# Kernel optimization log

Measured on AMD Instinct MI355X. Metric: run time of the kernel, lower is better.

## Reference

```python
import jax, jax.numpy as jnp
import numpy as np

N, E, F_IN, H, EF, G, GFD = 50000, 800000, 64, 128, 8, 10, 2
NEG_SLOPE = 0.2  # PyG GATv2Conv default negative_slope


def _gatv2_layer(x, src, dst, edge_attr, Wl, bl, Wr, br, We, att, bias):
    # PyG GATv2Conv, heads=1, concat=True, share_weights=False
    n = x.shape[0]
    xl = x @ Wl + bl            # source transform [N,H]
    xr = x @ Wr + br            # target transform [N,H]
    e = edge_attr @ We          # edge embedding   [E,H]
    s = jax.nn.leaky_relu(xl[src] + xr[dst] + e, NEG_SLOPE)  # [E,H]
    logits = s @ att            # [E]
    # numerically-stable segment softmax over destination nodes
    mx = jax.ops.segment_max(logits, dst, num_segments=n)
    mx = jnp.where(jnp.isfinite(mx), mx, 0.0)
    ex = jnp.exp(logits - mx[dst])
    den = jax.ops.segment_sum(ex, dst, num_segments=n)
    alpha = ex / jnp.maximum(den[dst], 1e-16)
    out = jax.ops.segment_sum(alpha[:, None] * xl[src], dst, num_segments=n)
    return out + bias


def _forward(x, edge_index, edge_attr, graph_features, num_graphs, params, head_W, head_b):
    src, dst = edge_index[0], edge_index[1]
    for (Wl, bl, Wr, br, We, att, bias) in params:
        x = jax.nn.relu(_gatv2_layer(x, src, dst, edge_attr, Wl, bl, Wr, br, We, att, bias))
        # dropout p=0.0 / eval mode: no-op
    n_nodes = x.shape[0] // num_graphs
    # faithful replication of the torch reshape chain (graph_feature_dim == 2):
    # graph_features.T [GFD,G] -> unsqueeze(2) -> repeat to [GFD,G,Np] -> view(G,GFD,Np)
    # -> cat(unbind(0), dim=1) -> [GFD, G*Np]
    gf = jnp.broadcast_to(graph_features.T[:, :, None], (GFD, num_graphs, n_nodes))
    gf = gf.reshape(num_graphs, GFD, n_nodes)
    gf = gf.transpose(1, 0, 2).reshape(GFD, num_graphs * n_nodes)
    x = jnp.concatenate([x, gf.T], axis=1)  # [N, H+GFD]
    return x @ head_W + head_b


def setup_inputs():
    key = jax.random.key(0)
    ks = list(jax.random.split(key, 32))
    p = lambda k, s: jax.random.normal(k, s, jnp.float32) * 0.05
    inp = {
        'x': jax.random.normal(ks[0], (N, F_IN), jnp.float32),
        'edge_index': jax.random.randint(ks[1], (2, E), 0, N),
        'edge_attr': jax.random.normal(ks[2], (E, EF), jnp.float32),
        'graph_features': jax.random.normal(ks[3], (G, GFD), jnp.float32),
        'num_graphs': G,
    }
    i = 4
    for l in range(3):
        fin = F_IN if l == 0 else H
        inp[f'Wl{l}'] = p(ks[i], (fin, H)); i += 1
        inp[f'bl{l}'] = jnp.zeros((H,), jnp.float32)
        inp[f'Wr{l}'] = p(ks[i], (fin, H)); i += 1
        inp[f'br{l}'] = jnp.zeros((H,), jnp.float32)
        inp[f'We{l}'] = p(ks[i], (EF, H)); i += 1
        inp[f'att{l}'] = p(ks[i], (H,)); i += 1
        inp[f'bias{l}'] = jnp.zeros((H,), jnp.float32)
    inp['head_W'] = p(ks[i], (H + GFD, 1))
    inp['head_b'] = jnp.zeros((1,), jnp.float32)
    return inp


def reference(x, edge_index, edge_attr, graph_features, num_graphs,
              Wl0, bl0, Wr0, br0, We0, att0, bias0,
              Wl1, bl1, Wr1, br1, We1, att1, bias1,
              Wl2, bl2, Wr2, br2, We2, att2, bias2,
              head_W, head_b):
    params = [(Wl0, bl0, Wr0, br0, We0, att0, bias0),
              (Wl1, bl1, Wr1, br1, We1, att1, bias1),
              (Wl2, bl2, Wr2, br2, We2, att2, bias2)]
    return _forward(x, edge_index, edge_attr, graph_features, num_graphs, params, head_W, head_b)
```

## Files before the change

kernel.cpp:

```cpp
#include <hip/hip_runtime.h>
#include <hip/hip_bf16.h>
#include <math.h>

#define NN 50000
#define EE 800000
#define F_IN 64
#define HH 128
#define EF 8
#define GG 10
#define GFD 2
#define NEG_SLOPE 0.2f
#define NB 64

__device__ __forceinline__ void fma4(float4& a, float s, const float4& b) {
  a.x = fmaf(s, b.x, a.x); a.y = fmaf(s, b.y, a.y);
  a.z = fmaf(s, b.z, a.z); a.w = fmaf(s, b.w, a.w);
}
__device__ __forceinline__ float lrelu1(float x) {
  return fmaxf(x, NEG_SLOPE * x);
}

template <int CTRL>
__device__ __forceinline__ float dpp_add(float v) {
  int p = __builtin_amdgcn_update_dpp(0, __float_as_int(v), CTRL, 0xf, 0xf, true);
  return v + __int_as_float(p);
}
__device__ __forceinline__ float red32(float v) {
  v = dpp_add<0xB1>(v);
  v = dpp_add<0x4E>(v);
  v = dpp_add<0x141>(v);
  v = dpp_add<0x140>(v);
  v += __int_as_float(__builtin_amdgcn_ds_swizzle(__float_as_int(v), 0x401F));
  return v;
}

__global__ __launch_bounds__(256) void lin2_kernel(
    const float* __restrict__ x, int fin,
    const float* __restrict__ Wl, const float* __restrict__ bl,
    const float* __restrict__ Wr, const float* __restrict__ br,
    float* __restrict__ xl, float* __restrict__ xr, int n_nodes) {
  __shared__ float xs[64 * 128];
  const int tid = threadIdx.x;
  const int base = blockIdx.x * 64;
  int nrows = n_nodes - base; if (nrows > 64) nrows = 64;

  const int total4 = (nrows * fin) >> 2;
  const float4* xsrc = (const float4*)(x + (size_t)base * fin);
  float4* xd = (float4*)xs;
  for (int i = tid; i < total4; i += 256) xd[i] = xsrc[i];
  __syncthreads();

  const int lane = tid & 63;
  const int w = tid >> 6;
  const int c = lane * 2;

  float accl0[16], accl1[16], accr0[16], accr1[16];
#pragma unroll
  for (int j = 0; j < 16; j++) { accl0[j]=0.f; accl1[j]=0.f; accr0[j]=0.f; accr1[j]=0.f; }

  const float* xrow = xs + (w * 16) * fin;
  for (int k = 0; k < fin; k += 2) {
    float2 wl0 = *(const float2*)(Wl + (size_t)k * HH + c);
    float2 wl1 = *(const float2*)(Wl + (size_t)(k + 1) * HH + c);
    float2 wr0 = *(const float2*)(Wr + (size_t)k * HH + c);
    float2 wr1 = *(const float2*)(Wr + (size_t)(k + 1) * HH + c);
#pragma unroll
    for (int j = 0; j < 16; j++) {
      float2 xv = *(const float2*)(xrow + j * fin + k);
      accl0[j] = fmaf(xv.x, wl0.x, accl0[j]);
      accl1[j] = fmaf(xv.x, wl0.y, accl1[j]);
      accr0[j] = fmaf(xv.x, wr0.x, accr0[j]);
      accr1[j] = fmaf(xv.x, wr0.y, accr1[j]);
      accl0[j] = fmaf(xv.y, wl1.x, accl0[j]);
      accl1[j] = fmaf(xv.y, wl1.y, accl1[j]);
      accr0[j] = fmaf(xv.y, wr1.x, accr0[j]);
      accr1[j] = fmaf(xv.y, wr1.y, accr1[j]);
    }
  }
  float2 blv = *(const float2*)(bl + c);
  float2 brv = *(const float2*)(br + c);
#pragma unroll
  for (int j = 0; j < 16; j++) {
    int n = base + w * 16 + j;
    if (n < n_nodes) {
      *(float2*)(xl + (size_t)n * HH + c) = make_float2(accl0[j] + blv.x, accl1[j] + blv.y);
      *(float2*)(xr + (size_t)n * HH + c) = make_float2(accr0[j] + brv.x, accr1[j] + brv.y);
    }
  }
}

__global__ __launch_bounds__(256) void hist_kernel(const int* __restrict__ dst,
                                                   int* __restrict__ hist, int ne) {
  int i = blockIdx.x * blockDim.x + threadIdx.x;
  if (i < ne) atomicAdd(&hist[dst[i]], 1);
}

__global__ __launch_bounds__(1024) void reduce_kernel(const int* __restrict__ hist,
                                                      int* __restrict__ bsum, int n) {
  __shared__ int wsum[16];
  const int tid = threadIdx.x;
  const int lane = tid & 63, w = tid >> 6;
  int i = blockIdx.x * 1024 + tid;
  int v = (i < n) ? hist[i] : 0;
#pragma unroll
  for (int off = 32; off; off >>= 1) v += __shfl_xor(v, off);
  if (lane == 0) wsum[w] = v;
  __syncthreads();
  if (tid < 16) {
    int s = wsum[tid];
#pragma unroll
    for (int off = 8; off; off >>= 1) s += __shfl_xor(s, off);
    if (tid == 0) bsum[blockIdx.x] = s;
  }
}

__global__ __launch_bounds__(64) void scanb_kernel(const int* __restrict__ bsum,
                                                   int* __restrict__ bbase,
                                                   int* __restrict__ offs, int nb, int n) {
  const int tid = threadIdx.x;
  int v = (tid < nb) ? bsum[tid] : 0;
  int inc = v;
#pragma unroll
  for (int d = 1; d < 64; d <<= 1) {
    int t2 = __shfl_up(inc, d);
    if (tid >= d) inc += t2;
  }
  if (tid < nb) bbase[tid] = inc - v;
  if (tid == 63) offs[n] = inc;
}

__global__ __launch_bounds__(1024) void scanc_kernel(const int* __restrict__ hist,
                                                     const int* __restrict__ bbase,
                                                     int* __restrict__ offs,
                                                     int* __restrict__ cursor, int n) {
  __shared__ int wsum[16], wpre[16];
  const int tid = threadIdx.x;
  const int lane = tid & 63, w = tid >> 6;
  int i = blockIdx.x * 1024 + tid;
  int orig = (i < n) ? hist[i] : 0;
  int v = orig;
#pragma unroll
  for (int d = 1; d < 64; d <<= 1) {
    int t2 = __shfl_up(v, d);
    if (lane >= d) v += t2;
  }
  if (lane == 63) wsum[w] = v;
  __syncthreads();
  if (tid < 16) {
    int s = wsum[tid];
    int inc = s;
#pragma unroll
    for (int d = 1; d < 16; d <<= 1) {
      int t2 = __shfl_up(inc, d);
      if (tid >= d) inc += t2;
    }
    wpre[tid] = inc - s;
  }
  __syncthreads();
  if (i < n) {
    int ex = bbase[blockIdx.x] + wpre[w] + (v - orig);
    offs[i] = ex; cursor[i] = ex;
  }
}

__global__ __launch_bounds__(256) void scatter_kernel(
    const int* __restrict__ src, const int* __restrict__ dst,
    int* __restrict__ cursor, int* __restrict__ pk,
    const float4* __restrict__ ea4, float4* __restrict__ eas, int ne) {
  int i = blockIdx.x * blockDim.x + threadIdx.x;
  if (i < ne) {
    int d = dst[i];
    int pos = atomicAdd(&cursor[d], 1);
    pk[pos] = src[i] * 512;
    float4 a = ea4[i * 2], b = ea4[i * 2 + 1];
    eas[pos * 2] = a; eas[pos * 2 + 1] = b;
  }
}

__global__ __launch_bounds__(256) void deg_hist_kernel(const int* __restrict__ offs,
                                                       int* __restrict__ hist2, int n) {
  __shared__ int lhist[NB];
  const int tid = threadIdx.x;
  int i = blockIdx.x * 256 + tid;
  if (tid < NB) lhist[tid] = 0;
  __syncthreads();
  if (i < n) {
    int d = offs[i + 1] - offs[i];
    int key = NB - 1 - min(d, NB - 1);
    atomicAdd(&lhist[key], 1);
  }
  __syncthreads();
  if (tid < NB && lhist[tid]) atomicAdd(&hist2[tid], lhist[tid]);
}

__global__ __launch_bounds__(64) void scan64_kernel(const int* __restrict__ hist2,
                                                    int* __restrict__ cursor2) {
  const int tid = threadIdx.x;
  int v = hist2[tid];
  int inc = v;
#pragma unroll
  for (int d = 1; d < 64; d <<= 1) {
    int t2 = __shfl_up(inc, d);
    if (tid >= d) inc += t2;
  }
  cursor2[tid] = inc - v;
}

__global__ __launch_bounds__(256) void deg_scatter_kernel(const int* __restrict__ offs,
                                                          int* __restrict__ cursor2,
                                                          int* __restrict__ nperm, int n) {
  __shared__ int lhist[NB];
  __shared__ int lbase[NB];
  const int tid = threadIdx.x;
  int i = blockIdx.x * 256 + tid;
  if (tid < NB) lhist[tid] = 0;
  __syncthreads();
  int key = 0, rank = 0;
  const bool valid = (i < n);
  if (valid) {
    int d = offs[i + 1] - offs[i];
    key = NB - 1 - min(d, NB - 1);
    rank = atomicAdd(&lhist[key], 1);
  }
  __syncthreads();
  if (tid < NB && lhist[tid]) lbase[tid] = atomicAdd(&cursor2[tid], lhist[tid]);
  __syncthreads();
  if (valid) nperm[lbase[key] + rank] = i;
}

__global__ __launch_bounds__(256, 4) void gat_fused_kernel(
    const float* __restrict__ xl, const float* __restrict__ xr,
    const float* __restrict__ eas, const float* __restrict__ We,
    const float* __restrict__ att,
    const int* __restrict__ pk, const int* __restrict__ offs,
    const int* __restrict__ nperm, const float* __restrict__ bias,
    float* __restrict__ xout, int n_nodes,
    float* __restrict__ out_head, const float* __restrict__ hw,
    const float* __restrict__ hb) {
  const int lane = threadIdx.x & 63;
  const int g = lane >> 5, t = lane & 31;
  const int c = t * 4;
  const int tb = t * 16;
  const int nwaves = gridDim.x * 4;

  float4 we[EF];
#pragma unroll
  for (int k = 0; k < EF; k++) we[k] = *(const float4*)(We + k * HH + c);
  const float4 at = *(const float4*)(att + c);
  const float4 bi = *(const float4*)(bias + c);
  const char* xlb = (const char*)xl;
  const char* easb = (const char*)eas;
  float4 hwv = make_float4(0.f, 0.f, 0.f, 0.f);
  float hw0 = 0.f, hw1 = 0.f, hb0 = 0.f;
  if (out_head) {
    hwv = *(const float4*)(hw + c);
    hw0 = hw[HH]; hw1 = hw[HH + 1]; hb0 = hb[0];
  }

  for (int wid = blockIdx.x * 4 + (threadIdx.x >> 6); wid < n_nodes; wid += nwaves) {
    const int node = nperm[wid];
    const int b = offs[node], e = offs[node + 1];
    const int deg = e - b;

    float4 o;
    if (deg == 0) {
      o.x = fmaxf(bi.x, 0.f); o.y = fmaxf(bi.y, 0.f);
      o.z = fmaxf(bi.z, 0.f); o.w = fmaxf(bi.w, 0.f);
    } else {
      const float4 vr = *(const float4*)(xr + (size_t)node * HH + c);
      const int emax = e - 1;

      float4 acc = make_float4(0.f, 0.f, 0.f, 0.f);
      float den = 0.f;
      float4 vlA, eaPA, eaQA, vlB, eaPB, eaQB;

#define LOADS(VL, EP, EQ, IDX)                                      \
  do {                                                              \
    int _cx = min((IDX), emax);                                     \
    EP = *(const float4*)(easb + (_cx << 5));                       \
    EQ = *(const float4*)(easb + (_cx << 5) + 16);                  \
    int _ob = pk[_cx];                                              \
    VL = *(const float4*)(xlb + (_ob + tb));                        \
  } while (0)

#define PROCESS(VL, EP, EQ, IDX)                                     \
  do {                                                               \
    float4 s = make_float4(VL.x + vr.x, VL.y + vr.y, VL.z + vr.z,    \
                           VL.w + vr.w);                             \
    fma4(s, EP.x, we[0]); fma4(s, EP.y, we[1]);                      \
    fma4(s, EP.z, we[2]); fma4(s, EP.w, we[3]);                      \
    fma4(s, EQ.x, we[4]); fma4(s, EQ.y, we[5]);                      \
    fma4(s, EQ.z, we[6]); fma4(s, EQ.w, we[7]);                      \
    float v = lrelu1(s.x) * at.x;                                    \
    v = fmaf(lrelu1(s.y), at.y, v);                                  \
    v = fmaf(lrelu1(s.z), at.z, v);                                  \
    v = fmaf(lrelu1(s.w), at.w, v);                                  \
    v = red32(v);                                                    \
    const float p = ((IDX) < e) ? __expf(v) : 0.f;                   \
    den += p;                                                        \
    fma4(acc, p, VL);                                                \
  } while (0)

      int idx = b + g;
      LOADS(vlA, eaPA, eaQA, idx);
      LOADS(vlB, eaPB, eaQB, idx + 2);

      const int nit = (deg + 3) >> 2;
      for (int j = 0; j < nit; j++) {
        PROCESS(vlA, eaPA, eaQA, idx);
        LOADS(vlA, eaPA, eaQA, idx + 4);
        PROCESS(vlB, eaPB, eaQB, idx + 2);
        LOADS(vlB, eaPB, eaQB, idx + 6);
        idx += 4;
      }
#undef LOADS
#undef PROCESS

      den += __shfl_xor(den, 32);
      acc.x += __shfl_xor(acc.x, 32);
      acc.y += __shfl_xor(acc.y, 32);
      acc.z += __shfl_xor(acc.z, 32);
      acc.w += __shfl_xor(acc.w, 32);

      const float inv = 1.f / fmaxf(den, 1e-16f);
      o.x = fmaxf(fmaf(acc.x, inv, bi.x), 0.f);
      o.y = fmaxf(fmaf(acc.y, inv, bi.y), 0.f);
      o.z = fmaxf(fmaf(acc.z, inv, bi.z), 0.f);
      o.w = fmaxf(fmaf(acc.w, inv, bi.w), 0.f);
    }

    if (!out_head) {
      if (g == 0) *(float4*)(xout + (size_t)node * HH + c) = o;
    } else {
      float hv = o.x * hwv.x + o.y * hwv.y + o.z * hwv.z + o.w * hwv.w;
      hv = red32(hv);
      if (lane == 0) {
        int k = node / (NN / GG);
        int i0 = 2 * k, i1 = 2 * k + 1;
        float g0 = hw0 * ((const float*)out_head == nullptr ? 0.f : 1.f);
        g0 = __ldg(&((const float*)hb)[0]);
        (void)g0;
        float gf0 = xout[(i0 % GG) * GFD + (i0 / GG)];
        float gf1 = xout[(i1 % GG) * GFD + (i1 / GG)];
        out_head[node] = hv + gf0 * hw0 + gf1 * hw1 + hb0;
      }
    }
  }
}

extern "C" void kernel_launch(void* const* d_in, const int* in_sizes, int n_in,
                              void* d_out, int out_size, void* d_ws, size_t ws_size,
                              hipStream_t stream) {
  const float* x_in = (const float*)d_in[0];
  const int*   eidx = (const int*)d_in[1];
  const float* ea   = (const float*)d_in[2];
  const float* gf   = (const float*)d_in[3];
  const int* src = eidx;
  const int* dst = eidx + EE;
  const float* head_W = (const float*)d_in[26];
  const float* head_b = (const float*)d_in[27];
  float* out = (float*)d_out;

  const int NCHUNK = (NN + 1023) / 1024;

  float* P      = (float*)d_ws;
  float* Q      = P + (size_t)NN * HH;
  float* R      = Q + (size_t)NN * HH;
  float* eas    = R + (size_t)NN * HH;
  int*   pk     = (int*)(eas + (size_t)EE * EF);
  int*   hist   = pk + EE;
  int*   offs   = hist + NN;
  int*   cursor = offs + NN + 1;
  int*   hist2  = cursor + NN;
  int*   cursor2= hist2 + NB;
  int*   nperm  = cursor2 + NB;
  int*   bsum   = nperm + NN;
  int*   bbase  = bsum + NCHUNK;

  (void)hipMemsetAsync(hist, 0, NN * sizeof(int), stream);
  (void)hipMemsetAsync(hist2, 0, NB * sizeof(int), stream);
  hist_kernel<<<(EE + 255) / 256, 256, 0, stream>>>(dst, hist, EE);
  reduce_kernel<<<NCHUNK, 1024, 0, stream>>>(hist, bsum, NN);
  scanb_kernel<<<1, 64, 0, stream>>>(bsum, bbase, offs, NCHUNK, NN);
  scanc_kernel<<<NCHUNK, 1024, 0, stream>>>(hist, bbase, offs, cursor, NN);
  scatter_kernel<<<(EE + 255) / 256, 256, 0, stream>>>(src, dst, cursor, pk,
                                                       (const float4*)ea, (float4*)eas, EE);
  deg_hist_kernel<<<(NN + 255) / 256, 256, 0, stream>>>(offs, hist2, NN);
  scan64_kernel<<<1, 64, 0, stream>>>(hist2, cursor2);
  deg_scatter_kernel<<<(NN + 255) / 256, 256, 0, stream>>>(offs, cursor2, nperm, NN);

  const float* xcur = x_in;
  int fin = F_IN;
  for (int l = 0; l < 3; l++) {
    const float* Wl   = (const float*)d_in[5 + 7 * l + 0];
    const float* bl   = (const float*)d_in[5 + 7 * l + 1];
    const float* Wr   = (const float*)d_in[5 + 7 * l + 2];
    const float* br   = (const float*)d_in[5 + 7 * l + 3];
    const float* We   = (const float*)d_in[5 + 7 * l + 4];
    const float* att  = (const float*)d_in[5 + 7 * l + 5];
    const float* bias = (const float*)d_in[5 + 7 * l + 6];

    lin2_kernel<<<(NN + 63) / 64, 256, 0, stream>>>(xcur, fin, Wl, bl, Wr, br, P, Q, NN);
    if (l < 2) {
      gat_fused_kernel<<<2048, 256, 0, stream>>>(P, Q, eas, We, att, pk, offs, nperm,
                                                 bias, R, NN, nullptr, nullptr, nullptr);
    } else {
      gat_fused_kernel<<<2048, 256, 0, stream>>>(P, Q, eas, We, att, pk, offs, nperm,
                                                 bias, (float*)gf, NN, out, head_W, head_b);
    }
    xcur = R;
    fin = HH;
  }
}
```

Before: 506.3 us.

## Pack node metadata into int4 and prefetch next node's data in GAT loop

```diff
diff --git a/kernel.cpp b/kernel.cpp
--- a/kernel.cpp
+++ b/kernel.cpp
@@ -59,14 +59,18 @@
   for (int j = 0; j < 16; j++) { accl0[j]=0.f; accl1[j]=0.f; accr0[j]=0.f; accr1[j]=0.f; }
 
   const float* xrow = xs + (w * 16) * fin;
-  for (int k = 0; k < fin; k += 2) {
+  for (int k = 0; k < fin; k += 4) {
     float2 wl0 = *(const float2*)(Wl + (size_t)k * HH + c);
     float2 wl1 = *(const float2*)(Wl + (size_t)(k + 1) * HH + c);
+    float2 wl2 = *(const float2*)(Wl + (size_t)(k + 2) * HH + c);
+    float2 wl3 = *(const float2*)(Wl + (size_t)(k + 3) * HH + c);
     float2 wr0 = *(const float2*)(Wr + (size_t)k * HH + c);
     float2 wr1 = *(const float2*)(Wr + (size_t)(k + 1) * HH + c);
+    float2 wr2 = *(const float2*)(Wr + (size_t)(k + 2) * HH + c);
+    float2 wr3 = *(const float2*)(Wr + (size_t)(k + 3) * HH + c);
 #pragma unroll
     for (int j = 0; j < 16; j++) {
-      float2 xv = *(const float2*)(xrow + j * fin + k);
+      float4 xv = *(const float4*)(xrow + j * fin + k);
       accl0[j] = fmaf(xv.x, wl0.x, accl0[j]);
       accl1[j] = fmaf(xv.x, wl0.y, accl1[j]);
       accr0[j] = fmaf(xv.x, wr0.x, accr0[j]);
@@ -75,6 +79,14 @@
       accl1[j] = fmaf(xv.y, wl1.y, accl1[j]);
       accr0[j] = fmaf(xv.y, wr1.x, accr0[j]);
       accr1[j] = fmaf(xv.y, wr1.y, accr1[j]);
+      accl0[j] = fmaf(xv.z, wl2.x, accl0[j]);
+      accl1[j] = fmaf(xv.z, wl2.y, accl1[j]);
+      accr0[j] = fmaf(xv.z, wr2.x, accr0[j]);
+      accr1[j] = fmaf(xv.z, wr2.y, accr1[j]);
+      accl0[j] = fmaf(xv.w, wl3.x, accl0[j]);
+      accl1[j] = fmaf(xv.w, wl3.y, accl1[j]);
+      accr0[j] = fmaf(xv.w, wr3.x, accr0[j]);
+      accr1[j] = fmaf(xv.w, wr3.y, accr1[j]);
     }
   }
   float2 blv = *(const float2*)(bl + c);
@@ -208,32 +220,33 @@
 
 __global__ __launch_bounds__(256) void deg_scatter_kernel(const int* __restrict__ offs,
                                                           int* __restrict__ cursor2,
-                                                          int* __restrict__ nperm, int n) {
+                                                          int4* __restrict__ meta4, int n) {
   __shared__ int lhist[NB];
   __shared__ int lbase[NB];
   const int tid = threadIdx.x;
   int i = blockIdx.x * 256 + tid;
   if (tid < NB) lhist[tid] = 0;
   __syncthreads();
-  int key = 0, rank = 0;
+  int key = 0, rank = 0, bb = 0, ee = 0;
   const bool valid = (i < n);
   if (valid) {
-    int d = offs[i + 1] - offs[i];
+    bb = offs[i]; ee = offs[i + 1];
+    int d = ee - bb;
     key = NB - 1 - min(d, NB - 1);
     rank = atomicAdd(&lhist[key], 1);
   }
   __syncthreads();
   if (tid < NB && lhist[tid]) lbase[tid] = atomicAdd(&cursor2[tid], lhist[tid]);
   __syncthreads();
-  if (valid) nperm[lbase[key] + rank] = i;
+  if (valid) meta4[lbase[key] + rank] = make_int4(bb, ee, i, 0);
 }
 
 __global__ __launch_bounds__(256, 4) void gat_fused_kernel(
     const float* __restrict__ xl, const float* __restrict__ xr,
     const float* __restrict__ eas, const float* __restrict__ We,
     const float* __restrict__ att,
-    const int* __restrict__ pk, const int* __restrict__ offs,
-    const int* __restrict__ nperm, const float* __restrict__ bias,
+    const int* __restrict__ pk, const int4* __restrict__ meta4,
+    const float* __restrict__ bias,
     float* __restrict__ xout, int n_nodes,
     float* __restrict__ out_head, const float* __restrict__ hw,
     const float* __restrict__ hb) {
@@ -257,19 +270,25 @@
     hw0 = hw[HH]; hw1 = hw[HH + 1]; hb0 = hb[0];
   }
 
-  for (int wid = blockIdx.x * 4 + (threadIdx.x >> 6); wid < n_nodes; wid += nwaves) {
-    const int node = nperm[wid];
-    const int b = offs[node], e = offs[node + 1];
+  int wid = blockIdx.x * 4 + (threadIdx.x >> 6);
+  if (wid >= n_nodes) return;
+  int4 mt = meta4[wid];
+  float4 vr = *(const float4*)(xr + (size_t)mt.z * HH + c);
+
+  while (true) {
+    const int b = mt.x, e = mt.y, node = mt.z;
     const int deg = e - b;
+    const int nwid = wid + nwaves;
+    const bool hasN = nwid < n_nodes;
+    int4 mtN = mt;
+    if (hasN) mtN = meta4[nwid];
 
     float4 o;
     if (deg == 0) {
       o.x = fmaxf(bi.x, 0.f); o.y = fmaxf(bi.y, 0.f);
       o.z = fmaxf(bi.z, 0.f); o.w = fmaxf(bi.w, 0.f);
     } else {
-      const float4 vr = *(const float4*)(xr + (size_t)node * HH + c);
       const int emax = e - 1;
-
       float4 acc = make_float4(0.f, 0.f, 0.f, 0.f);
       float den = 0.f;
       float4 vlA, eaPA, eaQA, vlB, eaPB, eaQB;
@@ -329,6 +348,9 @@
       o.w = fmaxf(fmaf(acc.w, inv, bi.w), 0.f);
     }
 
+    float4 vrN = vr;
+    if (hasN) vrN = *(const float4*)(xr + (size_t)mtN.z * HH + c);
+
     if (!out_head) {
       if (g == 0) *(float4*)(xout + (size_t)node * HH + c) = o;
     } else {
@@ -337,14 +359,14 @@
       if (lane == 0) {
         int k = node / (NN / GG);
         int i0 = 2 * k, i1 = 2 * k + 1;
-        float g0 = hw0 * ((const float*)out_head == nullptr ? 0.f : 1.f);
-        g0 = __ldg(&((const float*)hb)[0]);
-        (void)g0;
         float gf0 = xout[(i0 % GG) * GFD + (i0 / GG)];
         float gf1 = xout[(i1 % GG) * GFD + (i1 / GG)];
         out_head[node] = hv + gf0 * hw0 + gf1 * hw1 + hb0;
       }
     }
+
+    if (!hasN) break;
+    wid = nwid; mt = mtN; vr = vrN;
   }
 }
 
@@ -373,9 +395,9 @@
   int*   cursor = offs + NN + 1;
   int*   hist2  = cursor + NN;
   int*   cursor2= hist2 + NB;
-  int*   nperm  = cursor2 + NB;
-  int*   bsum   = nperm + NN;
+  int*   bsum   = cursor2 + NB;
   int*   bbase  = bsum + NCHUNK;
+  int4*  meta4  = (int4*)(((size_t)(bbase + NCHUNK) + 15) & ~(size_t)15);
 
   (void)hipMemsetAsync(hist, 0, NN * sizeof(int), stream);
   (void)hipMemsetAsync(hist2, 0, NB * sizeof(int), stream);
@@ -387,7 +409,7 @@
                                                        (const float4*)ea, (float4*)eas, EE);
   deg_hist_kernel<<<(NN + 255) / 256, 256, 0, stream>>>(offs, hist2, NN);
   scan64_kernel<<<1, 64, 0, stream>>>(hist2, cursor2);
-  deg_scatter_kernel<<<(NN + 255) / 256, 256, 0, stream>>>(offs, cursor2, nperm, NN);
+  deg_scatter_kernel<<<(NN + 255) / 256, 256, 0, stream>>>(offs, cursor2, meta4, NN);
 
   const float* xcur = x_in;
   int fin = F_IN;
@@ -402,10 +424,10 @@
 
     lin2_kernel<<<(NN + 63) / 64, 256, 0, stream>>>(xcur, fin, Wl, bl, Wr, br, P, Q, NN);
     if (l < 2) {
-      gat_fused_kernel<<<2048, 256, 0, stream>>>(P, Q, eas, We, att, pk, offs, nperm,
+      gat_fused_kernel<<<2048, 256, 0, stream>>>(P, Q, eas, We, att, pk, meta4,
                                                  bias, R, NN, nullptr, nullptr, nullptr);
     } else {
-      gat_fused_kernel<<<2048, 256, 0, stream>>>(P, Q, eas, We, att, pk, offs, nperm,
+      gat_fused_kernel<<<2048, 256, 0, stream>>>(P, Q, eas, We, att, pk, meta4,
                                                  bias, (float*)gf, NN, out, head_W, head_b);
     }
     xcur = R;
```

After: 494.5 us. 2.3% less time.
